# Performance work log

Hardware: AMD Instinct MI355X
Metric: run time of the kernel (lower is better)

The kernel has to match this reference:

```python
import jax, jax.numpy as jnp
import numpy as np

EPS_LN = 1e-5
EPS_W = 1e-16
K = 3


def layernorm(x, gamma, beta):
    mu = x.mean(-1, keepdims=True)
    var = ((x - mu) ** 2).mean(-1, keepdims=True)
    return (x - mu) * jax.lax.rsqrt(var + EPS_LN) * gamma + beta


def knn_interp(xb, pos_x, pos_y, k=K):
    """Inverse-squared-distance kNN interpolation.
    xb: [B, Nx, C] source features; pos_x: [Nx, 3]; pos_y: [Ny, 3].
    Positions are identical across batch (torch code expands them), so the
    kNN search is done once and the gather is broadcast over batch.
    Returns [B, Ny, C]."""
    # squared distances via ||y||^2 + ||x||^2 - 2 y.x  -> [Ny, Nx]
    d2 = ((pos_y * pos_y).sum(-1)[:, None]
          + (pos_x * pos_x).sum(-1)[None, :]
          - 2.0 * pos_y @ pos_x.T)
    _, idx = jax.lax.top_k(-d2, k)                      # [Ny, k] nearest
    # exact squared distances for the selected neighbors (matches torch math)
    diff = pos_x[idx] - pos_y[:, None, :]               # [Ny, k, 3]
    w = 1.0 / jnp.clip((diff * diff).sum(-1), EPS_W)    # [Ny, k]
    xg = xb[:, idx, :]                                  # [B, Ny, k, C]
    num = (xg * w[None, :, :, None]).sum(2)             # [B, Ny, C]
    return num / w.sum(1)[None, :, None]


def setup_inputs() -> dict:
    key = jax.random.key(0)
    k1, k2, k3 = jax.random.split(key, 3)
    B, N_MESH, N_PIV, C = 4, 40000, 2000, 128
    return {
        "node_features": jax.random.normal(k1, (B * N_MESH, C), jnp.float32),
        "gamma": jnp.ones((C,), jnp.float32),
        "beta": jnp.zeros((C,), jnp.float32),
        "position_mesh": jax.random.uniform(k2, (N_MESH, 3), jnp.float32),
        "position_pivotal": jax.random.uniform(k3, (N_PIV, 3), jnp.float32),
        "batch_size": 4,
    }


def reference(node_features, gamma, beta, position_mesh, position_pivotal, batch_size):
    B = batch_size
    C = node_features.shape[-1]
    Nm = position_mesh.shape[0]
    # encode: PivotalNorm then mesh -> pivotal interpolation
    h = layernorm(node_features, gamma, beta)
    hb = h.reshape(B, Nm, C)
    piv = knn_interp(hb, position_mesh, position_pivotal, K)      # [B, Npiv, C]
    # decode: pivotal -> mesh interpolation
    mesh = knn_interp(piv, position_pivotal, position_mesh, K)    # [B, Nm, C]
    return mesh.reshape(B * Nm, C)
```

## Files before the change

### kernel.cpp

```cpp
#include <hip/hip_runtime.h>
#include <hip/hip_bf16.h>
#include <math.h>

#define EPS_LN 1e-5f
#define EPS_W  1e-16f

__device__ __forceinline__ float cvt(const __hip_bfloat16 v) { return __bfloat162float(v); }
__device__ __forceinline__ float cvt(const float v)          { return v; }

__device__ __forceinline__ void load2(const __hip_bfloat16* p, float& a, float& b) {
    union { unsigned u; __hip_bfloat16 h[2]; } t;
    t.u = *(const unsigned*)p;
    a = __bfloat162float(t.h[0]); b = __bfloat162float(t.h[1]);
}
__device__ __forceinline__ void load2(const float* p, float& a, float& b) {
    float2 v = *(const float2*)p; a = v.x; b = v.y;
}

__device__ __forceinline__ void ins3lex(float nd, int ni, float d[3], int ix[3]) {
    bool b2 = (nd < d[2]) || (nd == d[2] && ni < ix[2]);
    if (!b2) return;
    bool b1 = (nd < d[1]) || (nd == d[1] && ni < ix[1]);
    bool b0 = (nd < d[0]) || (nd == d[0] && ni < ix[0]);
    if (b0)      { d[2]=d[1]; ix[2]=ix[1]; d[1]=d[0]; ix[1]=ix[0]; d[0]=nd; ix[0]=ni; }
    else if (b1) { d[2]=d[1]; ix[2]=ix[1]; d[1]=nd; ix[1]=ni; }
    else         { d[2]=nd; ix[2]=ni; }
}

__global__ __launch_bounds__(256)
void stage_kernel(const void* pmesh, int Nm, const void* ppiv, int Np,
                  float4* __restrict__ mesh_s, float4* __restrict__ piv_s,
                  int* __restrict__ flag) {
    __shared__ int sbad;
    if (threadIdx.x == 0) sbad = 0;
    __syncthreads();
    {
        const __hip_bfloat16* pb = (const __hip_bfloat16*)ppiv;
        int bad = 0;
        for (int i = threadIdx.x; i < Np * 3; i += 256) {
            float v = __bfloat162float(pb[i]);
            if (!(v >= 0.0f && v <= 1.0f)) bad = 1;
        }
        if (bad) sbad = 1;
    }
    __syncthreads();
    const int isf32 = sbad;

    int gid = blockIdx.x * 256 + threadIdx.x;
    if (gid == 0) *flag = isf32;
    const int total = Nm + Np;
    if (gid >= total) return;
    const int isMesh = gid < Nm ? 1 : 0;
    const int idx = isMesh ? gid : gid - Nm;
    const void* src = isMesh ? pmesh : ppiv;
    float x, y, z;
    if (isf32) {
        const float* p = (const float*)src;
        x = p[idx*3+0]; y = p[idx*3+1]; z = p[idx*3+2];
    } else {
        const __hip_bfloat16* p = (const __hip_bfloat16*)src;
        x = cvt(p[idx*3+0]); y = cvt(p[idx*3+1]); z = cvt(p[idx*3+2]);
    }
    float4 o; o.x = x; o.y = y; o.z = z; o.w = x*x + y*y + z*z;
    (isMesh ? mesh_s : piv_s)[idx] = o;
}

__global__ __launch_bounds__(256)
void knn_scan_kernel(const float4* __restrict__ cand, int Nc,
                     const float4* __restrict__ qry, int Nq,
                     int nslice, int chunk,
                     int* __restrict__ idx_out, float* __restrict__ wn_out,
                     float2* __restrict__ partials) {
    __shared__ float  sd[4][64][3];
    __shared__ int    si[4][64][3];

    const int tid   = threadIdx.x;
    const int lane  = tid & 63;
    const int wv    = __builtin_amdgcn_readfirstlane(tid >> 6);
    const int qg    = blockIdx.x / nslice;
    const int slice = blockIdx.x % nslice;
    const int q     = qg * 64 + lane;
    const int qc    = min(q, Nq - 1);

    const float4 qp = qry[qc];
    const float  qn = qp.w;

    float d0 = INFINITY, d1 = INFINITY, d2 = INFINITY;
    int   i0 = 0x7fffffff, i1 = 0x7fffffff, i2 = 0x7fffffff;

    const int jbeg = (slice * 4 + wv) * chunk;
    const int jend = min(jbeg + chunk, Nc);
    #pragma unroll 8
    for (int j = jbeg; j < jend; ++j) {
        const float4 cp = cand[j];
        float t   = qn + cp.w;
        float dot = qp.x*cp.x + qp.y*cp.y + qp.z*cp.z;
        float s   = t - 2.0f*dot;
        if (s < d2) {
            if (s < d1) {
                d2 = d1; i2 = i1;
                if (s < d0) { d1 = d0; i1 = i0; d0 = s; i0 = j; }
                else        { d1 = s;  i1 = j; }
            } else { d2 = s; i2 = j; }
        }
    }

    sd[wv][lane][0] = d0; sd[wv][lane][1] = d1; sd[wv][lane][2] = d2;
    si[wv][lane][0] = i0; si[wv][lane][1] = i1; si[wv][lane][2] = i2;
    __syncthreads();

    if (wv == 0) {
        float d[3]  = {d0, d1, d2};
        int   ix[3] = {i0, i1, i2};
        for (int w = 1; w < 4; ++w)
            for (int k = 0; k < 3; ++k)
                ins3lex(sd[w][lane][k], si[w][lane][k], d, ix);
        if (q < Nq) {
            if (nslice == 1) {
                float w_[3], ws = 0.f;
                for (int k = 0; k < 3; ++k) {
                    int ii = min(max(ix[k], 0), Nc - 1);
                    ix[k] = ii;
                    float4 cp = cand[ii];
                    float dx = cp.x - qp.x, dy = cp.y - qp.y, dz = cp.z - qp.z;
                    float dd = dx*dx + dy*dy + dz*dz;
                    w_[k] = 1.0f / fmaxf(dd, EPS_W);
                    ws += w_[k];
                }
                float inv = 1.0f / ws;
                for (int k = 0; k < 3; ++k) {
                    idx_out[q*3+k] = ix[k];
                    wn_out[q*3+k]  = w_[k] * inv;
                }
            } else {
                float2* p = partials + ((size_t)q * nslice + slice) * 3;
                for (int k = 0; k < 3; ++k) {
                    float2 e; e.x = d[k]; e.y = __int_as_float(ix[k]);
                    p[k] = e;
                }
            }
        }
    }
}

__global__ __launch_bounds__(256)
void knn_finalize_kernel(const float2* __restrict__ partials, int nslice,
                         const float4* __restrict__ cand, int Nc,
                         const float4* __restrict__ qry, int Nq,
                         int* __restrict__ idx_out, float* __restrict__ wn_out) {
    const int tid  = threadIdx.x;
    const int lane = tid & 63;
    const int q    = blockIdx.x * 4 + (tid >> 6);
    if (q >= Nq) return;

    const int nent = nslice * 3;
    const float2* p = partials + (size_t)q * nent;

    float d[3]  = {INFINITY, INFINITY, INFINITY};
    int   ix[3] = {0x7fffffff, 0x7fffffff, 0x7fffffff};
    for (int e = lane; e < nent; e += 64)
        ins3lex(p[e].x, __float_as_int(p[e].y), d, ix);

    #pragma unroll
    for (int off = 32; off >= 1; off >>= 1) {
        float od[3]; int oix[3];
        #pragma unroll
        for (int k = 0; k < 3; ++k) {
            od[k]  = __shfl_xor(d[k],  off);
            oix[k] = __shfl_xor(ix[k], off);
        }
        #pragma unroll
        for (int k = 0; k < 3; ++k) ins3lex(od[k], oix[k], d, ix);
    }

    if (lane == 0) {
        const float4 qp = qry[q];
        float w_[3], ws = 0.f;
        for (int k = 0; k < 3; ++k) {
            int ii = min(max(ix[k], 0), Nc - 1);
            ix[k] = ii;
            float4 cp = cand[ii];
            float dx = cp.x - qp.x, dy = cp.y - qp.y, dz = cp.z - qp.z;
            float dd = dx*dx + dy*dy + dz*dz;
            w_[k] = 1.0f / fmaxf(dd, EPS_W);
            ws += w_[k];
        }
        float inv = 1.0f / ws;
        for (int k = 0; k < 3; ++k) {
            idx_out[q*3+k] = ix[k];
            wn_out[q*3+k]  = w_[k] * inv;
        }
    }
}

template <typename T, typename S>
__device__ void interp_ln_wave_body(const T* __restrict__ xfeat,
                                    const T* __restrict__ gamma,
                                    const T* __restrict__ beta,
                                    const int* __restrict__ idx,
                                    const float* __restrict__ wn,
                                    S* __restrict__ piv,
                                    int Nm, int Np, int C, int B) {
    const int tid  = threadIdx.x;
    const int lane = tid & 63;
    const int wg   = blockIdx.x * 4 + (tid >> 6);
    if (wg >= B * Np) return;
    const int b  = wg / Np;
    const int j  = wg - b * Np;
    const int c0 = lane * 2;

    float g0, g1, be0, be1;
    load2(gamma + c0, g0, g1);
    load2(beta  + c0, be0, be1);

    const float invC = 1.0f / (float)C;
    float acc0 = 0.f, acc1 = 0.f;

    for (int k = 0; k < 3; ++k) {
        int row = idx[j*3+k];
        row = min(max(row, 0), Nm - 1);
        const T* xp = xfeat + ((size_t)b*Nm + row) * (size_t)C;
        float x0, x1;
        load2(xp + c0, x0, x1);
        float s  = x0 + x1;
        float s2 = x0*x0 + x1*x1;
        #pragma unroll
        for (int off = 32; off >= 1; off >>= 1) {
            s  += __shfl_xor(s,  off);
            s2 += __shfl_xor(s2, off);
        }
        float mean = s * invC;
        float var  = s2 * invC - mean*mean;
        float rs   = rsqrtf(var + EPS_LN);
        float wk   = wn[j*3+k];
        acc0 += wk * ((x0 - mean)*rs*g0 + be0);
        acc1 += wk * ((x1 - mean)*rs*g1 + be1);
    }

    S* pp = piv + ((size_t)b*Np + j) * (size_t)C + c0;
    if constexpr (sizeof(S) == 2) {
        union { S h[2]; unsigned u; } o;
        o.h[0] = __float2bfloat16(acc0);
        o.h[1] = __float2bfloat16(acc1);
        *(unsigned*)pp = o.u;
    } else {
        float2 o; o.x = acc0; o.y = acc1;
        *(float2*)pp = o;
    }
}

__global__ __launch_bounds__(256)
void interp_ln_wave_kernel(const void* xfeat, const void* gamma, const void* beta,
                           const int* idx, const float* wn, void* piv,
                           int Nm, int Np, int C, int B, const int* dtype_flag) {
    if (*dtype_flag)
        interp_ln_wave_body<float, float>((const float*)xfeat, (const float*)gamma,
                                          (const float*)beta, idx, wn,
                                          (float*)piv, Nm, Np, C, B);
    else
        interp_ln_wave_body<__hip_bfloat16, __hip_bfloat16>(
            (const __hip_bfloat16*)xfeat, (const __hip_bfloat16*)gamma,
            (const __hip_bfloat16*)beta, idx, wn,
            (__hip_bfloat16*)piv, Nm, Np, C, B);
}

template <typename T, typename S>
__device__ void interp_ln_body(const T* __restrict__ xfeat,
                               const T* __restrict__ gamma,
                               const T* __restrict__ beta,
                               const int* __restrict__ idx,
                               const float* __restrict__ wn,
                               S* __restrict__ piv, int Nm, int Np, int C) {
    const int j   = blockIdx.x % Np;
    const int b   = blockIdx.x / Np;
    const int c   = threadIdx.x;
    const int wid = c >> 6;
    const int nw  = C >> 6;

    const float g  = cvt(gamma[c]);
    const float be = cvt(beta[c]);

    __shared__ float red[8];
    float acc = 0.f;
    const float invC = 1.0f / (float)C;

    for (int k = 0; k < 3; ++k) {
        int row = idx[j*3+k];
        row = min(max(row, 0), Nm - 1);
        const T* xp = xfeat + ((size_t)b*Nm + row) * (size_t)C;
        float x = cvt(xp[c]);
        float s = x, s2 = x*x;
        for (int off = 32; off > 0; off >>= 1) {
            s  += __shfl_down(s,  off);
            s2 += __shfl_down(s2, off);
        }
        if ((c & 63) == 0) { red[wid] = s; red[4+wid] = s2; }
        __syncthreads();
        float sum = 0.f, sum2 = 0.f;
        for (int wv = 0; wv < nw; ++wv) { sum += red[wv]; sum2 += red[4+wv]; }
        float mean = sum * invC;
        float var  = sum2 * invC - mean*mean;
        float rs   = rsqrtf(var + EPS_LN);
        acc += wn[j*3+k] * ((x - mean)*rs*g + be);
        __syncthreads();
    }
    S ov; if constexpr (sizeof(S) == 2) ov = __float2bfloat16(acc); else ov = acc;
    piv[((size_t)b*Np + j) * (size_t)C + c] = ov;
}

__global__ __launch_bounds__(128)
void interp_ln_kernel(const void* xfeat, const void* gamma, const void* beta,
                      const int* idx, const float* wn, void* piv,
                      int Nm, int Np, int C, const int* dtype_flag) {
    if (*dtype_flag)
        interp_ln_body<float, float>((const float*)xfeat, (const float*)gamma,
                                     (const float*)beta, idx, wn,
                                     (float*)piv, Nm, Np, C);
    else
        interp_ln_body<__hip_bfloat16, __hip_bfloat16>(
            (const __hip_bfloat16*)xfeat, (const __hip_bfloat16*)gamma,
            (const __hip_bfloat16*)beta, idx, wn,
            (__hip_bfloat16*)piv, Nm, Np, C);
}

__global__ __launch_bounds__(256)
void gather_out_kernel(const void* __restrict__ pivv,
                       const int* __restrict__ idx, const float* __restrict__ wn,
                       void* __restrict__ out, int Nm, int Np, int C4,
                       int total4, const int* __restrict__ dtype_flag) {
    int gid = blockIdx.x * 256 + threadIdx.x;
    if (gid >= total4) return;
    int c4 = gid % C4;
    int r  = gid / C4;
    int i  = r % Nm;
    int b  = r / Nm;
    const int C = C4 * 4;
    int jj0 = min(max(idx[i*3+0], 0), Np - 1);
    int jj1 = min(max(idx[i*3+1], 0), Np - 1);
    int jj2 = min(max(idx[i*3+2], 0), Np - 1);
    float w0 = wn[i*3+0], w1 = wn[i*3+1], w2 = wn[i*3+2];

    if (*dtype_flag) {
        const float* pbase = (const float*)pivv + (size_t)b * Np * C;
        float4 v0 = *(const float4*)(pbase + (size_t)jj0 * C + c4*4);
        float4 v1 = *(const float4*)(pbase + (size_t)jj1 * C + c4*4);
        float4 v2 = *(const float4*)(pbase + (size_t)jj2 * C + c4*4);
        float4 o;
        o.x = w0*v0.x + w1*v1.x + w2*v2.x;
        o.y = w0*v0.y + w1*v1.y + w2*v2.y;
        o.z = w0*v0.z + w1*v1.z + w2*v2.z;
        o.w = w0*v0.w + w1*v1.w + w2*v2.w;
        *(((float4*)out) + gid) = o;
    } else {
        const __hip_bfloat16* pbase = (const __hip_bfloat16*)pivv + (size_t)b * Np * C;
        union { __hip_bfloat16 h[4]; uint2 v; } u0, u1, u2, o;
        u0.v = *(const uint2*)(pbase + (size_t)jj0 * C + c4*4);
        u1.v = *(const uint2*)(pbase + (size_t)jj1 * C + c4*4);
        u2.v = *(const uint2*)(pbase + (size_t)jj2 * C + c4*4);
        #pragma unroll
        for (int t = 0; t < 4; ++t) {
            float a = w0*cvt(u0.h[t]) + w1*cvt(u1.h[t]) + w2*cvt(u2.h[t]);
            o.h[t] = __float2bfloat16(a);
        }
        *(((uint2*)out) + gid) = o.v;
    }
}

__global__ void zero_words_kernel(unsigned* out, long long nwords) {
    long long i = (long long)blockIdx.x * 256 + threadIdx.x;
    if (i < nwords) out[i] = 0u;
}

extern "C" void kernel_launch(void* const* d_in, const int* in_sizes, int n_in,
                              void* d_out, int out_size, void* d_ws, size_t ws_size,
                              hipStream_t stream) {
    const int C  = in_sizes[1];
    const int Nm = in_sizes[3] / 3;
    const int Np = in_sizes[4] / 3;
    const int B  = in_sizes[0] / (Nm * C);

    const int nqg1 = (Np + 63) / 64;
    const int nqg2 = (Nm + 63) / 64;

    auto plan = [](int nqg, int Nc, int& nsl, int& chk) {
        nsl = (2048 + nqg - 1) / nqg;
        int maxsl = (Nc + 127) / 128;
        if (nsl > maxsl) nsl = maxsl;
        if (nsl < 1) nsl = 1;
        chk = (Nc + nsl*4 - 1) / (nsl*4);
    };
    int nsl1, chk1, nsl2, chk2;
    plan(nqg1, Nm, nsl1, chk1);
    plan(nqg2, Np, nsl2, chk2);

    size_t off = 0;
    size_t flag_o = 0, meshs_o = 0, pivs_o = 0, piv_o = 0;
    size_t i1_o = 0, w1_o = 0, i2_o = 0, w2_o = 0, p1_o = 0, p2_o = 0;
    auto layout = [&](int s1, int s2) {
        off = 0;
        auto carve = [&](size_t bytes) {
            size_t p = off;
            off += (bytes + 255) & ~(size_t)255;
            return p;
        };
        flag_o  = carve(256);
        meshs_o = carve((size_t)Nm * sizeof(float4));
        pivs_o  = carve((size_t)Np * sizeof(float4));
        piv_o   = carve((size_t)B * Np * C * sizeof(float));
        i1_o    = carve((size_t)Np * 3 * sizeof(int));
        w1_o    = carve((size_t)Np * 3 * sizeof(float));
        i2_o    = carve((size_t)Nm * 3 * sizeof(int));
        w2_o    = carve((size_t)Nm * 3 * sizeof(float));
        p1_o    = carve((size_t)Np * s1 * 3 * sizeof(float2));
        p2_o    = carve((size_t)Nm * s2 * 3 * sizeof(float2));
    };
    layout(nsl1, nsl2);
    if (off > ws_size) {
        nsl1 = 16; chk1 = (Nm + nsl1*4 - 1) / (nsl1*4);
        nsl2 = 1;  chk2 = (Np + nsl2*4 - 1) / (nsl2*4);
        layout(nsl1, nsl2);
    }
    if (off > ws_size) {
        long long nwords = (long long)out_size / 2;
        zero_words_kernel<<<(int)((nwords + 255) / 256), 256, 0, stream>>>(
            (unsigned*)d_out, nwords);
        return;
    }

    char* base = (char*)d_ws;
    int*    flag   = (int*)   (base + flag_o);
    float4* mesh_s = (float4*)(base + meshs_o);
    float4* piv_s  = (float4*)(base + pivs_o);
    void*   piv    = (void*)  (base + piv_o);
    int*    idx1   = (int*)   (base + i1_o);
    float*  wn1    = (float*) (base + w1_o);
    int*    idx2   = (int*)   (base + i2_o);
    float*  wn2    = (float*) (base + w2_o);
    float2* part1  = (float2*)(base + p1_o);
    float2* part2  = (float2*)(base + p2_o);

    stage_kernel<<<(Nm + Np + 255) / 256, 256, 0, stream>>>(
        d_in[3], Nm, d_in[4], Np, mesh_s, piv_s, flag);

    {
        knn_scan_kernel<<<nqg1 * nsl1, 256, 0, stream>>>(
            mesh_s, Nm, piv_s, Np, nsl1, chk1, idx1, wn1, part1);
        if (nsl1 > 1)
            knn_finalize_kernel<<<(Np + 3) / 4, 256, 0, stream>>>(
                part1, nsl1, mesh_s, Nm, piv_s, Np, idx1, wn1);
    }

    if (C == 128)
        interp_ln_wave_kernel<<<(B * Np + 3) / 4, 256, 0, stream>>>(
            d_in[0], d_in[1], d_in[2], idx1, wn1, piv, Nm, Np, C, B, flag);
    else
        interp_ln_kernel<<<B * Np, C, 0, stream>>>(d_in[0], d_in[1], d_in[2],
                                                   idx1, wn1, piv, Nm, Np, C, flag);

    {
        knn_scan_kernel<<<nqg2 * nsl2, 256, 0, stream>>>(
            piv_s, Np, mesh_s, Nm, nsl2, chk2, idx2, wn2, part2);
        if (nsl2 > 1)
            knn_finalize_kernel<<<(Nm + 3) / 4, 256, 0, stream>>>(
                part2, nsl2, piv_s, Np, mesh_s, Nm, idx2, wn2);
    }

    const int C4 = C / 4;
    const int total4 = B * Nm * C4;
    gather_out_kernel<<<(total4 + 255) / 256, 256, 0, stream>>>(
        piv, idx2, wn2, d_out, Nm, Np, C4, total4, flag);
}
```

Measured before the change: 273.8 us.

## Fuse both kNN scans into one launch and vectorize LN-interp and gather

Both kNN scans, and both finalize passes, now run in a single launch each, because the second search does not depend on the first interpolation. This cuts launch count and lets the two grids share the GPU. The LayerNorm-interp kernel now handles four rows per wave with 8-wide vector loads and shorter shuffle reductions. The output gather now loops over batch per thread with 8-wide loads, so the kNN indices and weights are reused across batches. The risk is load imbalance inside the fused grid and more register pressure.

```diff
diff --git a/kernel.cpp b/kernel.cpp
--- a/kernel.cpp
+++ b/kernel.cpp
@@ -8,13 +8,15 @@
 __device__ __forceinline__ float cvt(const __hip_bfloat16 v) { return __bfloat162float(v); }
 __device__ __forceinline__ float cvt(const float v)          { return v; }
 
-__device__ __forceinline__ void load2(const __hip_bfloat16* p, float& a, float& b) {
-    union { unsigned u; __hip_bfloat16 h[2]; } t;
-    t.u = *(const unsigned*)p;
-    a = __bfloat162float(t.h[0]); b = __bfloat162float(t.h[1]);
-}
-__device__ __forceinline__ void load2(const float* p, float& a, float& b) {
-    float2 v = *(const float2*)p; a = v.x; b = v.y;
+__device__ __forceinline__ void load8(const __hip_bfloat16* p, float* x) {
+    union { uint4 v; __hip_bfloat16 h[8]; } t;
+    t.v = *(const uint4*)p;
+    #pragma unroll
+    for (int i = 0; i < 8; ++i) x[i] = __bfloat162float(t.h[i]);
+}
+__device__ __forceinline__ void load8(const float* p, float* x) {
+    float4 a = *(const float4*)p, b = *(const float4*)(p + 4);
+    x[0]=a.x; x[1]=a.y; x[2]=a.z; x[3]=a.w; x[4]=b.x; x[5]=b.y; x[6]=b.z; x[7]=b.w;
 }
 
 __device__ __forceinline__ void ins3lex(float nd, int ni, float d[3], int ix[3]) {
@@ -65,20 +67,18 @@
     (isMesh ? mesh_s : piv_s)[idx] = o;
 }
 
-__global__ __launch_bounds__(256)
-void knn_scan_kernel(const float4* __restrict__ cand, int Nc,
-                     const float4* __restrict__ qry, int Nq,
-                     int nslice, int chunk,
-                     int* __restrict__ idx_out, float* __restrict__ wn_out,
-                     float2* __restrict__ partials) {
-    __shared__ float  sd[4][64][3];
-    __shared__ int    si[4][64][3];
-
+__device__ __forceinline__ void scan_body(
+        const float4* __restrict__ cand, int Nc,
+        const float4* __restrict__ qry, int Nq,
+        int blk, int nslice, int chunk,
+        int* __restrict__ idx_out, float* __restrict__ wn_out,
+        float2* __restrict__ partials,
+        float sd[4][64][3], int si[4][64][3]) {
     const int tid   = threadIdx.x;
     const int lane  = tid & 63;
     const int wv    = __builtin_amdgcn_readfirstlane(tid >> 6);
-    const int qg    = blockIdx.x / nslice;
-    const int slice = blockIdx.x % nslice;
+    const int qg    = blk / nslice;
+    const int slice = blk % nslice;
     const int q     = qg * 64 + lane;
     const int qc    = min(q, Nq - 1);
 
@@ -144,15 +144,30 @@
 }
 
 __global__ __launch_bounds__(256)
-void knn_finalize_kernel(const float2* __restrict__ partials, int nslice,
-                         const float4* __restrict__ cand, int Nc,
-                         const float4* __restrict__ qry, int Nq,
-                         int* __restrict__ idx_out, float* __restrict__ wn_out) {
-    const int tid  = threadIdx.x;
-    const int lane = tid & 63;
-    const int q    = blockIdx.x * 4 + (tid >> 6);
-    if (q >= Nq) return;
-
+void knn_scan_fused(const float4* __restrict__ mesh_s, int Nm,
+                    const float4* __restrict__ piv_s, int Np,
+                    int nb1, int nsl1, int chk1, int nsl2, int chk2,
+                    int* __restrict__ idx1, float* __restrict__ wn1,
+                    float2* __restrict__ part1,
+                    int* __restrict__ idx2, float* __restrict__ wn2,
+                    float2* __restrict__ part2) {
+    __shared__ float sd[4][64][3];
+    __shared__ int   si[4][64][3];
+    const int bid = blockIdx.x;
+    if (bid < nb1) {
+        scan_body(mesh_s, Nm, piv_s, Np, bid, nsl1, chk1,
+                  idx1, wn1, part1, sd, si);
+    } else {
+        scan_body(piv_s, Np, mesh_s, Nm, bid - nb1, nsl2, chk2,
+                  idx2, wn2, part2, sd, si);
+    }
+}
+
+__device__ __forceinline__ void finalize_wave(
+        const float2* __restrict__ partials, int nslice,
+        const float4* __restrict__ cand, int Nc,
+        const float4* __restrict__ qry, int q, int lane,
+        int* __restrict__ idx_out, float* __restrict__ wn_out) {
     const int nent = nslice * 3;
     const float2* p = partials + (size_t)q * nent;
 
@@ -193,39 +208,60 @@
     }
 }
 
+__global__ __launch_bounds__(256)
+void knn_finalize_fused(const float2* __restrict__ part1, int nsl1,
+                        const float4* __restrict__ mesh_s, int Nm,
+                        const float4* __restrict__ piv_s, int Np,
+                        const float2* __restrict__ part2, int nsl2,
+                        int nq1, int nq2,
+                        int* __restrict__ idx1, float* __restrict__ wn1,
+                        int* __restrict__ idx2, float* __restrict__ wn2) {
+    const int lane = threadIdx.x & 63;
+    const int w = blockIdx.x * 4 + (threadIdx.x >> 6);
+    if (w < nq1)
+        finalize_wave(part1, nsl1, mesh_s, Nm, piv_s, w, lane, idx1, wn1);
+    else if (w - nq1 < nq2)
+        finalize_wave(part2, nsl2, piv_s, Np, mesh_s, w - nq1, lane, idx2, wn2);
+}
+
 template <typename T, typename S>
-__device__ void interp_ln_wave_body(const T* __restrict__ xfeat,
-                                    const T* __restrict__ gamma,
-                                    const T* __restrict__ beta,
-                                    const int* __restrict__ idx,
-                                    const float* __restrict__ wn,
-                                    S* __restrict__ piv,
-                                    int Nm, int Np, int C, int B) {
+__device__ void interp_ln_wave4_body(const T* __restrict__ xfeat,
+                                     const T* __restrict__ gamma,
+                                     const T* __restrict__ beta,
+                                     const int* __restrict__ idx,
+                                     const float* __restrict__ wn,
+                                     S* __restrict__ piv,
+                                     int Nm, int Np, int C, int B) {
     const int tid  = threadIdx.x;
     const int lane = tid & 63;
-    const int wg   = blockIdx.x * 4 + (tid >> 6);
-    if (wg >= B * Np) return;
-    const int b  = wg / Np;
-    const int j  = wg - b * Np;
-    const int c0 = lane * 2;
-
-    float g0, g1, be0, be1;
-    load2(gamma + c0, g0, g1);
-    load2(beta  + c0, be0, be1);
+    const int sub  = lane >> 4;
+    const int l16  = lane & 15;
+    const int row_id = (blockIdx.x * 4 + (tid >> 6)) * 4 + sub;
+    if (row_id >= B * Np) return;
+    const int b  = row_id / Np;
+    const int j  = row_id - b * Np;
+    const int c0 = l16 * 8;
+
+    float g[8], be[8];
+    load8(gamma + c0, g);
+    load8(beta  + c0, be);
 
     const float invC = 1.0f / (float)C;
-    float acc0 = 0.f, acc1 = 0.f;
+    float acc[8];
+    #pragma unroll
+    for (int t = 0; t < 8; ++t) acc[t] = 0.f;
 
     for (int k = 0; k < 3; ++k) {
         int row = idx[j*3+k];
         row = min(max(row, 0), Nm - 1);
-        const T* xp = xfeat + ((size_t)b*Nm + row) * (size_t)C;
-        float x0, x1;
-        load2(xp + c0, x0, x1);
-        float s  = x0 + x1;
-        float s2 = x0*x0 + x1*x1;
-        #pragma unroll
-        for (int off = 32; off >= 1; off >>= 1) {
+        const T* xp = xfeat + ((size_t)b*Nm + row) * (size_t)C + c0;
+        float x[8];
+        load8(xp, x);
+        float s = 0.f, s2 = 0.f;
+        #pragma unroll
+        for (int t = 0; t < 8; ++t) { s += x[t]; s2 += x[t]*x[t]; }
+        #pragma unroll
+        for (int off = 8; off >= 1; off >>= 1) {
             s  += __shfl_xor(s,  off);
             s2 += __shfl_xor(s2, off);
         }
@@ -233,32 +269,36 @@
         float var  = s2 * invC - mean*mean;
         float rs   = rsqrtf(var + EPS_LN);
         float wk   = wn[j*3+k];
-        acc0 += wk * ((x0 - mean)*rs*g0 + be0);
-        acc1 += wk * ((x1 - mean)*rs*g1 + be1);
+        #pragma unroll
+        for (int t = 0; t < 8; ++t)
+            acc[t] += wk * ((x[t] - mean)*rs*g[t] + be[t]);
     }
 
     S* pp = piv + ((size_t)b*Np + j) * (size_t)C + c0;
     if constexpr (sizeof(S) == 2) {
-        union { S h[2]; unsigned u; } o;
-        o.h[0] = __float2bfloat16(acc0);
-        o.h[1] = __float2bfloat16(acc1);
-        *(unsigned*)pp = o.u;
-    } else {
-        float2 o; o.x = acc0; o.y = acc1;
-        *(float2*)pp = o;
+        union { uint4 v; S h[8]; } o;
+        #pragma unroll
+        for (int t = 0; t < 8; ++t) o.h[t] = __float2bfloat16(acc[t]);
+        *(uint4*)pp = o.v;
+    } else {
+        float4 a, c;
+        a.x = acc[0]; a.y = acc[1]; a.z = acc[2]; a.w = acc[3];
+        c.x = acc[4]; c.y = acc[5]; c.z = acc[6]; c.w = acc[7];
+        *(float4*)pp = a;
+        *(float4*)(pp + 4) = c;
     }
 }
 
 __global__ __launch_bounds__(256)
-void interp_ln_wave_kernel(const void* xfeat, const void* gamma, const void* beta,
-                           const int* idx, const float* wn, void* piv,
-                           int Nm, int Np, int C, int B, const int* dtype_flag) {
+void interp_ln_wave4_kernel(const void* xfeat, const void* gamma, const void* beta,
+                            const int* idx, const float* wn, void* piv,
+                            int Nm, int Np, int C, int B, const int* dtype_flag) {
     if (*dtype_flag)
-        interp_ln_wave_body<float, float>((const float*)xfeat, (const float*)gamma,
-                                          (const float*)beta, idx, wn,
-                                          (float*)piv, Nm, Np, C, B);
+        interp_ln_wave4_body<float, float>((const float*)xfeat, (const float*)gamma,
+                                           (const float*)beta, idx, wn,
+                                           (float*)piv, Nm, Np, C, B);
     else
-        interp_ln_wave_body<__hip_bfloat16, __hip_bfloat16>(
+        interp_ln_wave4_body<__hip_bfloat16, __hip_bfloat16>(
             (const __hip_bfloat16*)xfeat, (const __hip_bfloat16*)gamma,
             (const __hip_bfloat16*)beta, idx, wn,
             (__hip_bfloat16*)piv, Nm, Np, C, B);
@@ -321,6 +361,63 @@
             (const __hip_bfloat16*)xfeat, (const __hip_bfloat16*)gamma,
             (const __hip_bfloat16*)beta, idx, wn,
             (__hip_bfloat16*)piv, Nm, Np, C);
+}
+
+__global__ __launch_bounds__(256)
+void gather_out8_kernel(const void* __restrict__ pivv,
+                        const int* __restrict__ idx, const float* __restrict__ wn,
+                        void* __restrict__ out, int Nm, int Np, int C, int B,
+                        int total, const int* __restrict__ dtype_flag) {
+    int gid = blockIdx.x * 256 + threadIdx.x;
+    if (gid >= total) return;
+    const int C8 = C >> 3;
+    const int c8 = gid % C8;
+    const int i  = gid / C8;
+    int jj0 = min(max(idx[i*3+0], 0), Np - 1);
+    int jj1 = min(max(idx[i*3+1], 0), Np - 1);
+    int jj2 = min(max(idx[i*3+2], 0), Np - 1);
+    const float w0 = wn[i*3+0], w1 = wn[i*3+1], w2 = wn[i*3+2];
+    const int cb = c8 * 8;
+
+    if (*dtype_flag) {
+        const float* pv = (const float*)pivv;
+        float* po = (float*)out;
+        for (int b = 0; b < B; ++b) {
+            const float* pb = pv + (size_t)b * Np * C;
+            const float* r0 = pb + (size_t)jj0 * C + cb;
+            const float* r1 = pb + (size_t)jj1 * C + cb;
+            const float* r2 = pb + (size_t)jj2 * C + cb;
+            float* q = po + ((size_t)b*Nm + i) * (size_t)C + cb;
+            #pragma unroll
+            for (int h = 0; h < 2; ++h) {
+                float4 v0 = *(const float4*)(r0 + h*4);
+                float4 v1 = *(const float4*)(r1 + h*4);
+                float4 v2 = *(const float4*)(r2 + h*4);
+                float4 o;
+                o.x = w0*v0.x + w1*v1.x + w2*v2.x;
+                o.y = w0*v0.y + w1*v1.y + w2*v2.y;
+                o.z = w0*v0.z + w1*v1.z + w2*v2.z;
+                o.w = w0*v0.w + w1*v1.w + w2*v2.w;
+                *(float4*)(q + h*4) = o;
+            }
+        }
+    } else {
+        const __hip_bfloat16* pv = (const __hip_bfloat16*)pivv;
+        __hip_bfloat16* po = (__hip_bfloat16*)out;
+        for (int b = 0; b < B; ++b) {
+            const __hip_bfloat16* pb = pv + (size_t)b * Np * C;
+            union { uint4 v; __hip_bfloat16 h[8]; } u0, u1, u2, o;
+            u0.v = *(const uint4*)(pb + (size_t)jj0 * C + cb);
+            u1.v = *(const uint4*)(pb + (size_t)jj1 * C + cb);
+            u2.v = *(const uint4*)(pb + (size_t)jj2 * C + cb);
+            #pragma unroll
+            for (int t = 0; t < 8; ++t) {
+                float a = w0*cvt(u0.h[t]) + w1*cvt(u1.h[t]) + w2*cvt(u2.h[t]);
+                o.h[t] = __float2bfloat16(a);
+            }
+            *(uint4*)(po + ((size_t)b*Nm + i) * (size_t)C + cb) = o.v;
+        }
+    }
 }
 
 __global__ __launch_bounds__(256)
@@ -442,31 +539,36 @@
     stage_kernel<<<(Nm + Np + 255) / 256, 256, 0, stream>>>(
         d_in[3], Nm, d_in[4], Np, mesh_s, piv_s, flag);
 
-    {
-        knn_scan_kernel<<<nqg1 * nsl1, 256, 0, stream>>>(
-            mesh_s, Nm, piv_s, Np, nsl1, chk1, idx1, wn1, part1);
-        if (nsl1 > 1)
-            knn_finalize_kernel<<<(Np + 3) / 4, 256, 0, stream>>>(
-                part1, nsl1, mesh_s, Nm, piv_s, Np, idx1, wn1);
-    }
-
-    if (C == 128)
-        interp_ln_wave_kernel<<<(B * Np + 3) / 4, 256, 0, stream>>>(
+    const int nb1 = nqg1 * nsl1;
+    const int nb2 = nqg2 * nsl2;
+    knn_scan_fused<<<nb1 + nb2, 256, 0, stream>>>(
+        mesh_s, Nm, piv_s, Np, nb1, nsl1, chk1, nsl2, chk2,
+        idx1, wn1, part1, idx2, wn2, part2);
+
+    const int nq1 = (nsl1 > 1) ? Np : 0;
+    const int nq2 = (nsl2 > 1) ? Nm : 0;
+    if (nq1 + nq2 > 0)
+        knn_finalize_fused<<<(nq1 + nq2 + 3) / 4, 256, 0, stream>>>(
+            part1, nsl1, mesh_s, Nm, piv_s, Np, part2, nsl2,
+            nq1, nq2, idx1, wn1, idx2, wn2);
+
+    if (C == 128) {
+        const int nrow = B * Np;
+        interp_ln_wave4_kernel<<<(nrow + 15) / 16, 256, 0, stream>>>(
             d_in[0], d_in[1], d_in[2], idx1, wn1, piv, Nm, Np, C, B, flag);
-    else
+    } else {
         interp_ln_kernel<<<B * Np, C, 0, stream>>>(d_in[0], d_in[1], d_in[2],
                                                    idx1, wn1, piv, Nm, Np, C, flag);
-
-    {
-        knn_scan_kernel<<<nqg2 * nsl2, 256, 0, stream>>>(
-            piv_s, Np, mesh_s, Nm, nsl2, chk2, idx2, wn2, part2);
-        if (nsl2 > 1)
-            knn_finalize_kernel<<<(Nm + 3) / 4, 256, 0, stream>>>(
-                part2, nsl2, piv_s, Np, mesh_s, Nm, idx2, wn2);
-    }
-
-    const int C4 = C / 4;
-    const int total4 = B * Nm * C4;
-    gather_out_kernel<<<(total4 + 255) / 256, 256, 0, stream>>>(
-        piv, idx2, wn2, d_out, Nm, Np, C4, total4, flag);
-}
+    }
+
+    if ((C & 7) == 0) {
+        const int total = Nm * (C >> 3);
+        gather_out8_kernel<<<(total + 255) / 256, 256, 0, stream>>>(
+            piv, idx2, wn2, d_out, Nm, Np, C, B, total, flag);
+    } else {
+        const int C4 = C / 4;
+        const int total4 = B * Nm * C4;
+        gather_out_kernel<<<(total4 + 255) / 256, 256, 0, stream>>>(
+            piv, idx2, wn2, d_out, Nm, Np, C4, total4, flag);
+    }
+}
```

Measured after the change: 261.4 us. 4.5% less time.
